# Optimization experiments

Measured on AMD Instinct MI355X. Metric: run time of the kernel, lower is better.

The kernel has to match this reference:

```python
import jax, jax.numpy as jnp
import numpy as np

N = 2708       # hardcoded in the original forward (Cora)
INS = 1433
OUTS = 64
M = 8          # N_mechs
HID = 64       # conditioner hidden width
LEAK = 0.2
NEG = -1e9


def setup_inputs() -> dict:
    key = jax.random.key(0)
    ks = jax.random.split(key, 9)
    x = jax.random.normal(ks[0], (N, INS), dtype=jnp.float32)
    adj = jax.random.randint(ks[1], (N, N), 0, 2) > 0  # bool mask
    adj = adj | jnp.eye(N, dtype=bool)                 # ensure self-loops so softmax is well-defined
    s = 1.0 / np.sqrt(INS)
    W = jax.random.normal(ks[2], (M, INS, OUTS), dtype=jnp.float32) * s
    a_src = jax.random.normal(ks[3], (M, OUTS), dtype=jnp.float32) * (1.0 / np.sqrt(OUTS))
    a_dst = jax.random.normal(ks[4], (M, OUTS), dtype=jnp.float32) * (1.0 / np.sqrt(OUTS))
    Wc1 = jax.random.normal(ks[5], (INS, HID), dtype=jnp.float32) * s
    bc1 = jnp.zeros((HID,), dtype=jnp.float32)
    Wc2 = jax.random.normal(ks[6], (HID, 2 * M), dtype=jnp.float32) * (1.0 / np.sqrt(HID))
    bc2 = jnp.zeros((2 * M,), dtype=jnp.float32)
    return {"x": x, "adj": adj, "W": W, "a_src": a_src, "a_dst": a_dst,
            "Wc1": Wc1, "bc1": bc1, "Wc2": Wc2, "bc2": bc2}


def reference(x, adj, W, a_src, a_dst, Wc1, bc1, Wc2, bc2):
    # dropout is identity in eval mode.
    # Conditioner MLP applied per node (vectorized over the Python loop in the original):
    cond = jax.nn.relu(x @ Wc1 + bc1) @ Wc2 + bc2          # [N, 2M]
    c = cond.reshape(N, 2, M)                               # matches cond.view(2708, 2, -1)
    gamma = c[:, 0, :].T                                    # [M, N] per-node scalar gamma per mechanism
    beta = c[:, 1, :].T                                     # [M, N]
    # All mechanisms batched: project + FiLM modulate
    h = jnp.einsum('nf,mfo->mno', x, W)                     # [M, N, OUTS]
    h = gamma[:, :, None] * h + beta[:, :, None]
    # GAT scoring: e_ij = LeakyReLU(a_src.h_i + a_dst.h_j), masked by adj
    e_src = jnp.einsum('mno,mo->mn', h, a_src)              # [M, N]
    e_dst = jnp.einsum('mno,mo->mn', h, a_dst)              # [M, N]
    e = jax.nn.leaky_relu(e_src[:, :, None] + e_dst[:, None, :], LEAK)  # [M, N, N]
    e = jnp.where(adj[None, :, :], e, NEG)
    attn = jax.nn.softmax(e, axis=-1)                       # [M, N, N]
    out = jnp.einsum('mnk,mko->mno', attn, h)               # [M, N, OUTS]
    # concat=True: cat over mechanisms along feature dim
    out = jnp.transpose(out, (1, 0, 2)).reshape(N, M * OUTS)  # [N, M*OUTS]
    return out
```

## Files before the change

kernel.cpp:

```cpp
#include <hip/hip_runtime.h>

#define NN   2708
#define INS  1433
#define MM   8
#define NP   2720
#define WPR  85
#define KP   1440
#define NKC  45
#define RP   2752
#define C9   576
#define OC   512

#define CAN_ASRC 0
#define CAN_ADST 512
#define CAN_BC1  1024
#define CAN_BC2  1088
#define CAN_WC2  1104
#define CAN_TOT  2128

#define ADJ_WAVES (NN * 43)
#define ADJBLK ((ADJ_WAVES + 3) / 4)
#define XBLK   15480
#define WTBLK  (9 * 23)
#define PACK_TOT (ADJBLK + XBLK + WTBLK + 1)

typedef unsigned short u16;
typedef unsigned int   u32;
typedef __attribute__((ext_vector_type(8))) short bf16x8;
typedef __attribute__((ext_vector_type(4))) float f32x4;

static __device__ __forceinline__ u16 f2bfu(float f) {
    union { float f; u32 u; } v; v.f = f;
    u32 u = v.u;
    u32 r = (u + 0x7fffu + ((u >> 16) & 1u)) >> 16;
    return (u16)r;
}
static __device__ __forceinline__ float bfu2f(u16 b) {
    union { u32 u; float f; } v; v.u = ((u32)b) << 16;
    return v.f;
}

static __device__ __forceinline__ int xfp32_of(const int* ctr) {
    int s = 0;
    #pragma unroll
    for (int k = 0; k < 32; ++k) s += ctr[k];
    return s > 32;
}
static __device__ __forceinline__ int aflag_of(const int* ctr) {
    int b = 0;
    #pragma unroll
    for (int k = 32; k < 64; ++k) b |= ctr[k];
    if (b & 2)  return 3;
    if (b & 4)  return 4;
    if (b & 8)  return 5;
    if (b & 1)  return 1;
    if (b & 16) return 0;
    return 2;
}

__global__ void k_probe(const u32* __restrict__ x_raw, const u32* __restrict__ adj_raw,
                        int* __restrict__ ctr) {
    const int b = blockIdx.x, t = threadIdx.x;
    __shared__ int sred[4];
    if (b < 32) {
        int local = 0;
        #pragma unroll
        for (int k = 0; k < 8; ++k) {
            u32 v = x_raw[b * 2048 + k * 256 + t];
            u32 lo = v & 0xffffu, hi = v >> 16;
            if ((lo & 0x7f80u) == 0u && lo != 0u) local++;
            if ((hi & 0x7f80u) == 0u && hi != 0u) local++;
        }
        #pragma unroll
        for (int off = 32; off > 0; off >>= 1) local += __shfl_xor(local, off, 64);
        if ((t & 63) == 0) sred[t >> 6] = local;
        __syncthreads();
        if (t == 0) ctr[b] = sred[0] + sred[1] + sred[2] + sred[3];
    } else {
        int fl = 0;
        #pragma unroll
        for (int k = 0; k < 8; ++k) {
            int w = (b - 32) * 2048 + k * 256 + t;
            u32 v = adj_raw[w];
            if (v > 1u)           fl |= 1;
            if (v == 0x3f803f80u) fl |= 2;
            if (v == 0x3f800000u) fl |= 4;
            if (v == 0x3c003c00u) fl |= 8;
            if ((w & 1) && v)     fl |= 16;
        }
        #pragma unroll
        for (int off = 32; off > 0; off >>= 1) fl |= __shfl_xor(fl, off, 64);
        if ((t & 63) == 0) sred[t >> 6] = fl;
        __syncthreads();
        if (t == 0) ctr[b] = sred[0] | sred[1] | sred[2] | sred[3];
    }
}

static __device__ __forceinline__ u16 load_as_bf16(const void* p, size_t idx, int fp32) {
    if (fp32) return f2bfu(((const float*)p)[idx]);
    return ((const u16*)p)[idx];
}
static __device__ __forceinline__ float load_as_f32(const void* p, size_t idx, int fp32) {
    if (fp32) return ((const float*)p)[idx];
    return bfu2f(((const u16*)p)[idx]);
}

__global__ void k_pack(const void* __restrict__ x, const void* __restrict__ adj,
                       const void* __restrict__ W, const void* __restrict__ Wc1,
                       const void* a_src, const void* a_dst, const void* bc1,
                       const void* bc2, const void* Wc2,
                       u16* __restrict__ xpf, u16* __restrict__ WTf,
                       u32* __restrict__ adjT, float* __restrict__ canon,
                       const int* __restrict__ ctr) {
    __shared__ float lds[64][65];
    const int bid = blockIdx.x;
    if (bid < ADJBLK) {
        const int f = aflag_of(ctr);
        const int wid  = bid * 4 + (threadIdx.x >> 6);
        const int lane = threadIdx.x & 63;
        const int i  = wid / 43;
        const int jb = (wid - i * 43) * 64;
        if (i >= NN) return;
        const int j = jb + lane;
        int v = 0;
        if (j < NN) {
            size_t s = (size_t)i * NN + j;
            if      (f == 0) v = ((const int*)adj)[s] != 0;
            else if (f == 1) v = ((const unsigned char*)adj)[s] != 0;
            else if (f == 2) v = ((const long long*)adj)[s] != 0;
            else if (f == 4) v = ((const float*)adj)[s] != 0.f;
            else             v = ((const u16*)adj)[s] != 0;
        }
        unsigned long long mask = __ballot(v);
        if (lane == 0) {
            const int ww = jb >> 5;
            adjT[(size_t)ww * NP + i] = (u32)mask;
            if (ww + 1 < WPR) adjT[(size_t)(ww + 1) * NP + i] = (u32)(mask >> 32);
        }
    } else if (bid < ADJBLK + XBLK) {
        const int fp32 = xfp32_of(ctr);
        int e = (bid - ADJBLK) * 256 + threadIdx.x;
        int t1 = e >> 9, sub = e & 511;
        int r = sub >> 5, kloc = sub & 31;
        int it = t1 / NKC, kc = t1 - it * NKC;
        int row = it * 16 + r, col = kc * 32 + kloc;
        u16 v = 0;
        if (row < NN && col < INS) v = load_as_bf16(x, (size_t)row * INS + col, fp32);
        xpf[e] = v;
    } else if (bid < ADJBLK + XBLK + WTBLK) {
        const int fp32 = xfp32_of(ctr);
        const int b2 = bid - ADJBLK - XBLK;
        const int mblk = b2 / 23, ktile = b2 - mblk * 23;
        #pragma unroll
        for (int ii = 0; ii < 16; ++ii) {
            int l = threadIdx.x * 16 + ii;
            int k_in = l >> 6, o = l & 63;
            int k = ktile * 64 + k_in;
            float v = 0.f;
            if (k < INS) {
                if (mblk < 8) v = load_as_f32(W, ((size_t)mblk * INS + k) * 64 + o, fp32);
                else          v = load_as_f32(Wc1, (size_t)k * 64 + o, fp32);
            }
            lds[k_in][o] = v;
        }
        __syncthreads();
        #pragma unroll
        for (int ii = 0; ii < 16; ++ii) {
            int e2 = threadIdx.x * 16 + ii;
            int ct2 = e2 >> 10, kc2 = (e2 >> 9) & 1;
            int r = (e2 >> 5) & 15, kloc = e2 & 31;
            int kc = ktile * 2 + kc2;
            if (kc < NKC) {
                int ct = mblk * 4 + ct2;
                WTf[(((size_t)ct * NKC + kc) * 16 + r) * 32 + kloc] =
                    f2bfu(lds[kc2 * 32 + kloc][ct2 * 16 + r]);
            }
        }
    } else {
        const int fp32 = xfp32_of(ctr);
        for (int e = threadIdx.x; e < CAN_TOT; e += 256) {
            float v;
            if      (e < CAN_ADST) v = load_as_f32(a_src, e - CAN_ASRC, fp32);
            else if (e < CAN_BC1)  v = load_as_f32(a_dst, e - CAN_ADST, fp32);
            else if (e < CAN_BC2)  v = load_as_f32(bc1,  e - CAN_BC1, fp32);
            else if (e < CAN_WC2)  v = load_as_f32(bc2,  e - CAN_BC2, fp32);
            else                   v = load_as_f32(Wc2,  e - CAN_WC2, fp32);
            canon[e] = v;
        }
    }
}

__launch_bounds__(64)
__global__ void k_gemm(const u16* __restrict__ xpf, const u16* __restrict__ WTf,
                       float* __restrict__ h_pre) {
    const int lane = threadIdx.x;
    const int r    = lane & 15;
    const int quad = lane >> 4;
    const int it0  = blockIdx.x * 2;
    const int ct0  = blockIdx.y * 4;

    const u16* aP0 = xpf + (size_t)it0 * NKC * 512 + r * 32 + quad * 8;
    const u16* aP1 = aP0 + (size_t)NKC * 512;
    const u16* bP  = WTf + (size_t)ct0 * NKC * 512 + r * 32 + quad * 8;

    f32x4 acc0[4], acc1[4];
    #pragma unroll
    for (int nt = 0; nt < 4; ++nt) {
        acc0[nt] = (f32x4){0.f, 0.f, 0.f, 0.f};
        acc1[nt] = (f32x4){0.f, 0.f, 0.f, 0.f};
    }

    #pragma unroll 3
    for (int kc = 0; kc < NKC; ++kc) {
        bf16x8 a0 = *(const bf16x8*)(aP0 + kc * 512);
        bf16x8 a1 = *(const bf16x8*)(aP1 + kc * 512);
        #pragma unroll
        for (int nt = 0; nt < 4; ++nt) {
            bf16x8 bfr = *(const bf16x8*)(bP + (size_t)nt * NKC * 512 + kc * 512);
            acc0[nt] = __builtin_amdgcn_mfma_f32_16x16x32_bf16(a0, bfr, acc0[nt], 0, 0, 0);
            acc1[nt] = __builtin_amdgcn_mfma_f32_16x16x32_bf16(a1, bfr, acc1[nt], 0, 0, 0);
        }
    }

    const int c_base = blockIdx.y * 64;
    #pragma unroll
    for (int reg = 0; reg < 4; ++reg) {
        const int i0 = it0 * 16 + quad * 4 + reg;
        if (i0 < NN) {
            float* orow = h_pre + (size_t)i0 * C9 + c_base;
            orow[ 0 + r] = acc0[0][reg];
            orow[16 + r] = acc0[1][reg];
            orow[32 + r] = acc0[2][reg];
            orow[48 + r] = acc0[3][reg];
        }
        const int i1 = it0 * 16 + 16 + quad * 4 + reg;
        if (i1 < NN) {
            float* orow = h_pre + (size_t)i1 * C9 + c_base;
            orow[ 0 + r] = acc1[0][reg];
            orow[16 + r] = acc1[1][reg];
            orow[32 + r] = acc1[2][reg];
            orow[48 + r] = acc1[3][reg];
        }
    }
}

__launch_bounds__(256)
__global__ void k_film(const float* __restrict__ h_pre, const float* __restrict__ canon,
                       u16* __restrict__ HTf, float* __restrict__ e_srcP,
                       float* __restrict__ e_dstP) {
    const int m  = blockIdx.y;
    const int n0 = blockIdx.x * 32;
    const int t  = threadIdx.x, wave = t >> 6, o = t & 63;
    __shared__ u16 hbuf[32][66];

    const float wg = canon[CAN_WC2 + o * 16 + m];
    const float wb = canon[CAN_WC2 + o * 16 + m + 8];
    const float as = canon[CAN_ASRC + m * 64 + o];
    const float ad = canon[CAN_ADST + m * 64 + o];
    const float b1 = canon[CAN_BC1 + o];
    const float g0 = canon[CAN_BC2 + m], b0 = canon[CAN_BC2 + m + 8];

    #pragma unroll
    for (int it = 0; it < 8; ++it) {
        const int nl = wave * 8 + it, n = n0 + nl;
        const bool valid = n < NN;
        float hv = 0.f;
        if (valid) hv = h_pre[(size_t)n * C9 + 512 + o] + b1;
        hv = hv > 0.f ? hv : 0.f;
        float pg = hv * wg, pb = hv * wb;
        #pragma unroll
        for (int off = 32; off > 0; off >>= 1) {
            pg += __shfl_xor(pg, off, 64);
            pb += __shfl_xor(pb, off, 64);
        }
        const float g = pg + g0, bb = pb + b0;
        float h = 0.f;
        if (valid) h = g * h_pre[(size_t)n * C9 + m * 64 + o] + bb;
        float ps = h * as, pd = h * ad;
        #pragma unroll
        for (int off = 32; off > 0; off >>= 1) {
            ps += __shfl_xor(ps, off, 64);
            pd += __shfl_xor(pd, off, 64);
        }
        if (o == 0) { e_srcP[m * NP + n] = ps; e_dstP[m * NP + n] = pd; }
        hbuf[nl][o] = f2bfu(h);
    }
    __syncthreads();
    u32* ht32 = (u32*)(HTf + ((size_t)m * WPR + (n0 >> 5)) * 2048);
    #pragma unroll
    for (int rep = 0; rep < 4; ++rep) {
        const int idx = rep * 256 + t;
        const int oo = idx >> 4, jp = idx & 15;
        ht32[idx] = (u32)hbuf[2 * jp][oo] | ((u32)hbuf[2 * jp + 1][oo] << 16);
    }
}

__global__ void k_prep(const float* __restrict__ e_srcP, const float* __restrict__ e_dstP,
                       float* __restrict__ E1P, float* __restrict__ E2P,
                       float* __restrict__ F1P, float* __restrict__ F2P) {
    const int m = blockIdx.x, sl = blockIdx.y, t = threadIdx.x;
    const float* ed = e_dstP + m * NP;
    const float* es = e_srcP + m * NP;
    float mx = -3.0e38f;
    for (int j = t; j < NP; j += 256) mx = fmaxf(mx, ed[j]);
    #pragma unroll
    for (int off = 32; off > 0; off >>= 1) mx = fmaxf(mx, __shfl_xor(mx, off, 64));
    __shared__ float sm[4];
    if ((t & 63) == 0) sm[t >> 6] = mx;
    __syncthreads();
    const float maxd = fmaxf(fmaxf(sm[0], sm[1]), fmaxf(sm[2], sm[3]));
    const int j0 = sl * (NP / 8);
    for (int j = j0 + t; j < j0 + NP / 8; j += 256) {
        const float d = ed[j] - maxd;
        E1P[m * NP + j] = __expf(d);
        E2P[m * NP + j] = __expf(0.2f * d);
    }
    for (int i = j0 + t; i < j0 + NP / 8; i += 256) {
        const float v = es[i] + maxd;
        const float rmax = v > 0.f ? v : 0.2f * v;
        F1P[m * NP + i] = __expf(v - rmax);
        F2P[m * NP + i] = __expf(0.2f * v - rmax);
    }
}

__launch_bounds__(256)
__global__ void k_attn(const u32* __restrict__ adjT, const float* __restrict__ F1P,
                       const float* __restrict__ F2P, const float* __restrict__ E1P,
                       const float* __restrict__ E2P, const u16* __restrict__ HTf,
                       void* __restrict__ outv, const int* __restrict__ ctr) {
    const int m = blockIdx.y, i0 = blockIdx.x * 16;
    const int t = threadIdx.x;
    const int wave = t >> 6, lane = t & 63;
    const int r = lane & 15, quad = lane >> 4;
    const int i = min(i0 + r, NN - 1);

    __shared__ float sE[2 * NP];
    __shared__ u32 sAdj[WPR * 16];

    for (int idx = t; idx < NP; idx += 256) {
        sE[idx]      = E1P[m * NP + idx];
        sE[NP + idx] = E2P[m * NP + idx];
    }
    for (int w = t; w < WPR * 16; w += 256) {
        const int tile = w >> 4, rr = w & 15;
        sAdj[w] = adjT[(size_t)tile * NP + min(i0 + rr, NN - 1)];
    }
    __syncthreads();

    const float F1 = F1P[m * NP + i], F2 = F2P[m * NP + i];
    const u16* hbase = HTf + (size_t)m * WPR * 2048 + r * 32 + quad * 8;

    f32x4 acc[4], accl;
    #pragma unroll
    for (int nt = 0; nt < 4; ++nt) acc[nt] = (f32x4){0.f, 0.f, 0.f, 0.f};
    accl = (f32x4){0.f, 0.f, 0.f, 0.f};

    bf16x8 ones;
    #pragma unroll
    for (int kk = 0; kk < 8; ++kk) ones[kk] = (short)0x3f80;

    #pragma unroll 2
    for (int jc = wave * 32; jc < NP; jc += 128) {
        const int jb = jc + quad * 8;
        const int tile = jc >> 5;
        const float4 a0 = *(const float4*)(sE + jb);
        const float4 a1 = *(const float4*)(sE + jb + 4);
        const float4 b0 = *(const float4*)(sE + NP + jb);
        const float4 b1 = *(const float4*)(sE + NP + jb + 4);
        const u32 w = sAdj[tile * 16 + r];
        const u32 mask8 = (w >> (quad * 8)) & 0xffu;
        float p[8];
        p[0] = fmaxf(F1 * a0.x, F2 * b0.x);
        p[1] = fmaxf(F1 * a0.y, F2 * b0.y);
        p[2] = fmaxf(F1 * a0.z, F2 * b0.z);
        p[3] = fmaxf(F1 * a0.w, F2 * b0.w);
        p[4] = fmaxf(F1 * a1.x, F2 * b1.x);
        p[5] = fmaxf(F1 * a1.y, F2 * b1.y);
        p[6] = fmaxf(F1 * a1.z, F2 * b1.z);
        p[7] = fmaxf(F1 * a1.w, F2 * b1.w);
        bf16x8 af;
        #pragma unroll
        for (int kk = 0; kk < 8; ++kk) {
            const float pv = ((mask8 >> kk) & 1u) ? p[kk] : 0.f;
            af[kk] = (short)f2bfu(pv);
        }
        const u16* ht = hbase + (size_t)tile * 2048;
        #pragma unroll
        for (int nt = 0; nt < 4; ++nt) {
            bf16x8 bf = *(const bf16x8*)(ht + nt * 512);
            acc[nt] = __builtin_amdgcn_mfma_f32_16x16x32_bf16(af, bf, acc[nt], 0, 0, 0);
        }
        accl = __builtin_amdgcn_mfma_f32_16x16x32_bf16(af, ones, accl, 0, 0, 0);
    }

    __syncthreads();
    float* red = sE;
    #pragma unroll
    for (int nt = 0; nt < 4; ++nt)
        #pragma unroll
        for (int reg = 0; reg < 4; ++reg)
            red[(wave * 64 + lane) * 21 + nt * 4 + reg] = acc[nt][reg];
    #pragma unroll
    for (int reg = 0; reg < 4; ++reg)
        red[(wave * 64 + lane) * 21 + 16 + reg] = accl[reg];
    __syncthreads();
    if (wave != 0) return;

    #pragma unroll
    for (int nt = 0; nt < 4; ++nt)
        #pragma unroll
        for (int reg = 0; reg < 4; ++reg)
            acc[nt][reg] = red[lane * 21 + nt * 4 + reg] + red[(64 + lane) * 21 + nt * 4 + reg]
                         + red[(128 + lane) * 21 + nt * 4 + reg] + red[(192 + lane) * 21 + nt * 4 + reg];
    #pragma unroll
    for (int reg = 0; reg < 4; ++reg)
        accl[reg] = red[lane * 21 + 16 + reg] + red[(64 + lane) * 21 + 16 + reg]
                  + red[(128 + lane) * 21 + 16 + reg] + red[(192 + lane) * 21 + 16 + reg];

    const int ofp32 = xfp32_of(ctr);
    #pragma unroll
    for (int reg = 0; reg < 4; ++reg) {
        const int ii = i0 + quad * 4 + reg;
        if (ii < NN) {
            const float lr = accl[reg];
            const float inv = (lr > 0.f) ? 1.f / lr : 0.f;
            #pragma unroll
            for (int nt = 0; nt < 4; ++nt) {
                const float o = acc[nt][reg] * inv;
                const size_t idx = (size_t)ii * OC + m * 64 + nt * 16 + r;
                if (ofp32) ((float*)outv)[idx] = o;
                else       ((u16*)outv)[idx]   = f2bfu(o);
            }
        }
    }
}

extern "C" void kernel_launch(void* const* d_in, const int* in_sizes, int n_in,
                              void* d_out, int out_size, void* d_ws, size_t ws_size,
                              hipStream_t stream) {
    (void)in_sizes; (void)n_in; (void)out_size; (void)ws_size;
    const void* x     = d_in[0];
    const void* adj   = d_in[1];
    const void* W     = d_in[2];
    const void* a_src = d_in[3];
    const void* a_dst = d_in[4];
    const void* Wc1   = d_in[5];
    const void* bc1   = d_in[6];
    const void* Wc2   = d_in[7];
    const void* bc2   = d_in[8];

    char* ws = (char*)d_ws;
    size_t off = 0;
    auto alloc = [&](size_t bytes) -> void* {
        void* p = ws + off;
        off += (bytes + 255) & ~(size_t)255;
        return p;
    };
    u16*   xpf     = (u16*)  alloc((size_t)RP * KP * 2);
    u16*   WTf     = (u16*)  alloc((size_t)C9 * KP * 2);
    float* h_pre   = (float*)alloc((size_t)NN * C9 * 4);
    float* e_srcP  = (float*)alloc((size_t)MM * NP * 4);
    float* e_dstP  = (float*)alloc((size_t)MM * NP * 4);
    float* E1P     = (float*)alloc((size_t)MM * NP * 4);
    float* E2P     = (float*)alloc((size_t)MM * NP * 4);
    float* F1P     = (float*)alloc((size_t)MM * NP * 4);
    float* F2P     = (float*)alloc((size_t)MM * NP * 4);
    u16*   HTf     = (u16*)  alloc((size_t)MM * WPR * 2048 * 2);
    u32*   adjT    = (u32*)  alloc((size_t)WPR * NP * 4);
    float* canon   = (float*)alloc((size_t)CAN_TOT * 4);
    int*   ctr     = (int*)  alloc(256);

    hipLaunchKernelGGL(k_probe, dim3(64), dim3(256), 0, stream,
                       (const u32*)x, (const u32*)adj, ctr);
    hipLaunchKernelGGL(k_pack, dim3(PACK_TOT), dim3(256), 0, stream,
                       x, adj, W, Wc1, a_src, a_dst, bc1, bc2, Wc2,
                       xpf, WTf, adjT, canon, ctr);
    hipLaunchKernelGGL(k_gemm, dim3(RP / 32, 9), dim3(64), 0, stream, xpf, WTf, h_pre);
    hipLaunchKernelGGL(k_film, dim3(NP / 32, MM), dim3(256), 0, stream,
                       h_pre, canon, HTf, e_srcP, e_dstP);
    hipLaunchKernelGGL(k_prep, dim3(MM, 8), dim3(256), 0, stream,
                       e_srcP, e_dstP, E1P, E2P, F1P, F2P);
    hipLaunchKernelGGL(k_attn, dim3((NN + 15) / 16, MM), dim3(256), 0, stream,
                       adjT, F1P, F2P, E1P, E2P, HTf, d_out, ctr);
}
```

Baseline: 208.3 us.

## Process 32 rows per attention block with two wave groups sharing staged E

The attention kernel now uses 512-thread blocks covering 32 destination rows, split into two 4-wave groups of 16 rows each. Both groups share one shared-memory copy of the E1/E2 exponent vectors, which halves the redundant global loads and LDS staging per row. The cross-wave reduction is reworked so lane-group leaders keep their own accumulators and add the other three waves' partials. Larger blocks may lower occupancy flexibility, and the grid shrinks to 85x8 blocks, which could leave some compute units underused.

```diff
diff --git a/kernel.cpp b/kernel.cpp
--- a/kernel.cpp
+++ b/kernel.cpp
@@ -323,26 +323,29 @@
     }
 }
 
-__launch_bounds__(256)
+__launch_bounds__(512)
 __global__ void k_attn(const u32* __restrict__ adjT, const float* __restrict__ F1P,
                        const float* __restrict__ F2P, const float* __restrict__ E1P,
                        const float* __restrict__ E2P, const u16* __restrict__ HTf,
                        void* __restrict__ outv, const int* __restrict__ ctr) {
-    const int m = blockIdx.y, i0 = blockIdx.x * 16;
+    const int m = blockIdx.y, i0 = blockIdx.x * 32;
     const int t = threadIdx.x;
     const int wave = t >> 6, lane = t & 63;
+    const int grp = wave >> 2, wl = wave & 3;
     const int r = lane & 15, quad = lane >> 4;
-    const int i = min(i0 + r, NN - 1);
-
-    __shared__ float sE[2 * NP];
-    __shared__ u32 sAdj[WPR * 16];
-
-    for (int idx = t; idx < NP; idx += 256) {
+    const int ib = i0 + grp * 16;
+    const int i = min(ib + r, NN - 1);
+
+    __shared__ u32 smem[2 * NP + WPR * 32];
+    float* sE = (float*)smem;
+    u32* sAdj = smem + 2 * NP;
+
+    for (int idx = t; idx < NP; idx += 512) {
         sE[idx]      = E1P[m * NP + idx];
         sE[NP + idx] = E2P[m * NP + idx];
     }
-    for (int w = t; w < WPR * 16; w += 256) {
-        const int tile = w >> 4, rr = w & 15;
+    for (int w = t; w < WPR * 32; w += 512) {
+        const int tile = w >> 5, rr = w & 31;
         sAdj[w] = adjT[(size_t)tile * NP + min(i0 + rr, NN - 1)];
     }
     __syncthreads();
@@ -360,14 +363,14 @@
     for (int kk = 0; kk < 8; ++kk) ones[kk] = (short)0x3f80;
 
     #pragma unroll 2
-    for (int jc = wave * 32; jc < NP; jc += 128) {
+    for (int jc = wl * 32; jc < NP; jc += 128) {
         const int jb = jc + quad * 8;
         const int tile = jc >> 5;
         const float4 a0 = *(const float4*)(sE + jb);
         const float4 a1 = *(const float4*)(sE + jb + 4);
         const float4 b0 = *(const float4*)(sE + NP + jb);
         const float4 b1 = *(const float4*)(sE + NP + jb + 4);
-        const u32 w = sAdj[tile * 16 + r];
+        const u32 w = sAdj[tile * 32 + grp * 16 + r];
         const u32 mask8 = (w >> (quad * 8)) & 0xffu;
         float p[8];
         p[0] = fmaxf(F1 * a0.x, F2 * b0.x);
@@ -394,33 +397,38 @@
     }
 
     __syncthreads();
-    float* red = sE;
-    #pragma unroll
-    for (int nt = 0; nt < 4; ++nt)
+    float* red = (float*)smem;
+    if (wl != 0) {
+        float* dst = red + ((grp * 3 + (wl - 1)) * 64 + lane) * 21;
+        #pragma unroll
+        for (int nt = 0; nt < 4; ++nt)
+            #pragma unroll
+            for (int reg = 0; reg < 4; ++reg)
+                dst[nt * 4 + reg] = acc[nt][reg];
         #pragma unroll
         for (int reg = 0; reg < 4; ++reg)
-            red[(wave * 64 + lane) * 21 + nt * 4 + reg] = acc[nt][reg];
-    #pragma unroll
-    for (int reg = 0; reg < 4; ++reg)
-        red[(wave * 64 + lane) * 21 + 16 + reg] = accl[reg];
+            dst[16 + reg] = accl[reg];
+    }
     __syncthreads();
-    if (wave != 0) return;
-
-    #pragma unroll
-    for (int nt = 0; nt < 4; ++nt)
+    if (wl != 0) return;
+
+    #pragma unroll
+    for (int s = 0; s < 3; ++s) {
+        const float* src = red + ((grp * 3 + s) * 64 + lane) * 21;
+        #pragma unroll
+        for (int nt = 0; nt < 4; ++nt)
+            #pragma unroll
+            for (int reg = 0; reg < 4; ++reg)
+                acc[nt][reg] += src[nt * 4 + reg];
         #pragma unroll
         for (int reg = 0; reg < 4; ++reg)
-            acc[nt][reg] = red[lane * 21 + nt * 4 + reg] + red[(64 + lane) * 21 + nt * 4 + reg]
-                         + red[(128 + lane) * 21 + nt * 4 + reg] + red[(192 + lane) * 21 + nt * 4 + reg];
-    #pragma unroll
-    for (int reg = 0; reg < 4; ++reg)
-        accl[reg] = red[lane * 21 + 16 + reg] + red[(64 + lane) * 21 + 16 + reg]
-                  + red[(128 + lane) * 21 + 16 + reg] + red[(192 + lane) * 21 + 16 + reg];
+            accl[reg] += src[16 + reg];
+    }
 
     const int ofp32 = xfp32_of(ctr);
     #pragma unroll
     for (int reg = 0; reg < 4; ++reg) {
-        const int ii = i0 + quad * 4 + reg;
+        const int ii = ib + quad * 4 + reg;
         if (ii < NN) {
             const float lr = accl[reg];
             const float inv = (lr > 0.f) ? 1.f / lr : 0.f;
@@ -480,6 +488,6 @@
                        h_pre, canon, HTf, e_srcP, e_dstP);
     hipLaunchKernelGGL(k_prep, dim3(MM, 8), dim3(256), 0, stream,
                        e_srcP, e_dstP, E1P, E2P, F1P, F2P);
-    hipLaunchKernelGGL(k_attn, dim3((NN + 15) / 16, MM), dim3(256), 0, stream,
+    hipLaunchKernelGGL(k_attn, dim3(NP / 32, MM), dim3(512), 0, stream,
                        adjT, F1P, F2P, E1P, E2P, HTf, d_out, ctr);
 }
```

After: 213.6 us. +2.6%, slower.

## Coarsen pack kernel work per block and halve GEMM column tile for more blocks

Applied to the files above, without the earlier changes.

The pack kernel now reduces the probe flags once per block with wave shuffles into shared memory, instead of every thread looping over the counters. Each adjacency wave covers four 64-column chunks and each x-pack block handles eight elements per thread, which cuts the block count roughly fourfold and eightfold. The GEMM switches from a 2x4 to a 2x2 MFMA tile per wave and doubles the grid in y, giving more blocks for occupancy but reloading A fragments twice as often. The pack changes add a block-wide barrier before any work starts.

```diff
diff --git a/kernel.cpp b/kernel.cpp
--- a/kernel.cpp
+++ b/kernel.cpp
@@ -18,9 +18,9 @@
 #define CAN_WC2  1104
 #define CAN_TOT  2128
 
-#define ADJ_WAVES (NN * 43)
+#define ADJ_WAVES (NN * 11)
 #define ADJBLK ((ADJ_WAVES + 3) / 4)
-#define XBLK   15480
+#define XBLK   1935
 #define WTBLK  (9 * 23)
 #define PACK_TOT (ADJBLK + XBLK + WTBLK + 1)
 
@@ -46,10 +46,7 @@
     for (int k = 0; k < 32; ++k) s += ctr[k];
     return s > 32;
 }
-static __device__ __forceinline__ int aflag_of(const int* ctr) {
-    int b = 0;
-    #pragma unroll
-    for (int k = 32; k < 64; ++k) b |= ctr[k];
+static __device__ __forceinline__ int aflag_decode(int b) {
     if (b & 2)  return 3;
     if (b & 4)  return 4;
     if (b & 8)  return 5;
@@ -113,47 +110,71 @@
                        u32* __restrict__ adjT, float* __restrict__ canon,
                        const int* __restrict__ ctr) {
     __shared__ float lds[64][65];
+    __shared__ int sflags[2];
+    const int t = threadIdx.x;
+    if (t < 64) {
+        int v = ctr[t];
+        int cnt  = (t < 32) ? v : 0;
+        int bits = (t >= 32) ? v : 0;
+        #pragma unroll
+        for (int off = 32; off > 0; off >>= 1) {
+            cnt  += __shfl_xor(cnt, off, 64);
+            bits |= __shfl_xor(bits, off, 64);
+        }
+        if (t == 0) { sflags[0] = cnt; sflags[1] = bits; }
+    }
+    __syncthreads();
+    const int fp32 = sflags[0] > 32;
+
     const int bid = blockIdx.x;
     if (bid < ADJBLK) {
-        const int f = aflag_of(ctr);
-        const int wid  = bid * 4 + (threadIdx.x >> 6);
-        const int lane = threadIdx.x & 63;
-        const int i  = wid / 43;
-        const int jb = (wid - i * 43) * 64;
+        const int f = aflag_decode(sflags[1]);
+        const int wid  = bid * 4 + (t >> 6);
+        const int lane = t & 63;
+        const int i = wid / 11;
+        const int c256 = wid - i * 11;
         if (i >= NN) return;
-        const int j = jb + lane;
-        int v = 0;
-        if (j < NN) {
-            size_t s = (size_t)i * NN + j;
-            if      (f == 0) v = ((const int*)adj)[s] != 0;
-            else if (f == 1) v = ((const unsigned char*)adj)[s] != 0;
-            else if (f == 2) v = ((const long long*)adj)[s] != 0;
-            else if (f == 4) v = ((const float*)adj)[s] != 0.f;
-            else             v = ((const u16*)adj)[s] != 0;
-        }
-        unsigned long long mask = __ballot(v);
-        if (lane == 0) {
-            const int ww = jb >> 5;
-            adjT[(size_t)ww * NP + i] = (u32)mask;
-            if (ww + 1 < WPR) adjT[(size_t)(ww + 1) * NP + i] = (u32)(mask >> 32);
+        const int jb0 = c256 * 256;
+        #pragma unroll
+        for (int s = 0; s < 4; ++s) {
+            const int jb = jb0 + s * 64;
+            if (jb >= NP) break;
+            const int j = jb + lane;
+            int v = 0;
+            if (j < NN) {
+                size_t idx = (size_t)i * NN + j;
+                if      (f == 0) v = ((const int*)adj)[idx] != 0;
+                else if (f == 1) v = ((const unsigned char*)adj)[idx] != 0;
+                else if (f == 2) v = ((const long long*)adj)[idx] != 0;
+                else if (f == 4) v = ((const float*)adj)[idx] != 0.f;
+                else             v = ((const u16*)adj)[idx] != 0;
+            }
+            unsigned long long mask = __ballot(v);
+            if (lane == 0) {
+                const int ww = jb >> 5;
+                adjT[(size_t)ww * NP + i] = (u32)mask;
+                if (ww + 1 < WPR) adjT[(size_t)(ww + 1) * NP + i] = (u32)(mask >> 32);
+            }
         }
     } else if (bid < ADJBLK + XBLK) {
-        const int fp32 = xfp32_of(ctr);
-        int e = (bid - ADJBLK) * 256 + threadIdx.x;
-        int t1 = e >> 9, sub = e & 511;
-        int r = sub >> 5, kloc = sub & 31;
-        int it = t1 / NKC, kc = t1 - it * NKC;
-        int row = it * 16 + r, col = kc * 32 + kloc;
-        u16 v = 0;
-        if (row < NN && col < INS) v = load_as_bf16(x, (size_t)row * INS + col, fp32);
-        xpf[e] = v;
+        const int base = (bid - ADJBLK) * 2048 + t;
+        #pragma unroll
+        for (int s = 0; s < 8; ++s) {
+            const int e = base + s * 256;
+            const int t1 = e >> 9, sub = e & 511;
+            const int r = sub >> 5, kloc = sub & 31;
+            const int it = t1 / NKC, kc = t1 - it * NKC;
+            const int row = it * 16 + r, col = kc * 32 + kloc;
+            u16 v = 0;
+            if (row < NN && col < INS) v = load_as_bf16(x, (size_t)row * INS + col, fp32);
+            xpf[e] = v;
+        }
     } else if (bid < ADJBLK + XBLK + WTBLK) {
-        const int fp32 = xfp32_of(ctr);
         const int b2 = bid - ADJBLK - XBLK;
         const int mblk = b2 / 23, ktile = b2 - mblk * 23;
         #pragma unroll
         for (int ii = 0; ii < 16; ++ii) {
-            int l = threadIdx.x * 16 + ii;
+            int l = t * 16 + ii;
             int k_in = l >> 6, o = l & 63;
             int k = ktile * 64 + k_in;
             float v = 0.f;
@@ -166,7 +187,7 @@
         __syncthreads();
         #pragma unroll
         for (int ii = 0; ii < 16; ++ii) {
-            int e2 = threadIdx.x * 16 + ii;
+            int e2 = t * 16 + ii;
             int ct2 = e2 >> 10, kc2 = (e2 >> 9) & 1;
             int r = (e2 >> 5) & 15, kloc = e2 & 31;
             int kc = ktile * 2 + kc2;
@@ -177,8 +198,7 @@
             }
         }
     } else {
-        const int fp32 = xfp32_of(ctr);
-        for (int e = threadIdx.x; e < CAN_TOT; e += 256) {
+        for (int e = t; e < CAN_TOT; e += 256) {
             float v;
             if      (e < CAN_ADST) v = load_as_f32(a_src, e - CAN_ASRC, fp32);
             else if (e < CAN_BC1)  v = load_as_f32(a_dst, e - CAN_ADST, fp32);
@@ -197,49 +217,41 @@
     const int r    = lane & 15;
     const int quad = lane >> 4;
     const int it0  = blockIdx.x * 2;
-    const int ct0  = blockIdx.y * 4;
+    const int ct0  = blockIdx.y * 2;
 
     const u16* aP0 = xpf + (size_t)it0 * NKC * 512 + r * 32 + quad * 8;
     const u16* aP1 = aP0 + (size_t)NKC * 512;
-    const u16* bP  = WTf + (size_t)ct0 * NKC * 512 + r * 32 + quad * 8;
-
-    f32x4 acc0[4], acc1[4];
-    #pragma unroll
-    for (int nt = 0; nt < 4; ++nt) {
-        acc0[nt] = (f32x4){0.f, 0.f, 0.f, 0.f};
-        acc1[nt] = (f32x4){0.f, 0.f, 0.f, 0.f};
-    }
+    const u16* bP0 = WTf + (size_t)ct0 * NKC * 512 + r * 32 + quad * 8;
+    const u16* bP1 = bP0 + (size_t)NKC * 512;
+
+    f32x4 acc[2][2];
+    #pragma unroll
+    for (int a = 0; a < 2; ++a)
+        #pragma unroll
+        for (int b = 0; b < 2; ++b) acc[a][b] = (f32x4){0.f, 0.f, 0.f, 0.f};
 
     #pragma unroll 3
     for (int kc = 0; kc < NKC; ++kc) {
         bf16x8 a0 = *(const bf16x8*)(aP0 + kc * 512);
         bf16x8 a1 = *(const bf16x8*)(aP1 + kc * 512);
-        #pragma unroll
-        for (int nt = 0; nt < 4; ++nt) {
-            bf16x8 bfr = *(const bf16x8*)(bP + (size_t)nt * NKC * 512 + kc * 512);
-            acc0[nt] = __builtin_amdgcn_mfma_f32_16x16x32_bf16(a0, bfr, acc0[nt], 0, 0, 0);
-            acc1[nt] = __builtin_amdgcn_mfma_f32_16x16x32_bf16(a1, bfr, acc1[nt], 0, 0, 0);
-        }
-    }
-
-    const int c_base = blockIdx.y * 64;
-    #pragma unroll
-    for (int reg = 0; reg < 4; ++reg) {
-        const int i0 = it0 * 16 + quad * 4 + reg;
-        if (i0 < NN) {
-            float* orow = h_pre + (size_t)i0 * C9 + c_base;
-            orow[ 0 + r] = acc0[0][reg];
-            orow[16 + r] = acc0[1][reg];
-            orow[32 + r] = acc0[2][reg];
-            orow[48 + r] = acc0[3][reg];
-        }
-        const int i1 = it0 * 16 + 16 + quad * 4 + reg;
-        if (i1 < NN) {
-            float* orow = h_pre + (size_t)i1 * C9 + c_base;
-            orow[ 0 + r] = acc1[0][reg];
-            orow[16 + r] = acc1[1][reg];
-            orow[32 + r] = acc1[2][reg];
-            orow[48 + r] = acc1[3][reg];
+        bf16x8 b0 = *(const bf16x8*)(bP0 + kc * 512);
+        bf16x8 b1 = *(const bf16x8*)(bP1 + kc * 512);
+        acc[0][0] = __builtin_amdgcn_mfma_f32_16x16x32_bf16(a0, b0, acc[0][0], 0, 0, 0);
+        acc[0][1] = __builtin_amdgcn_mfma_f32_16x16x32_bf16(a0, b1, acc[0][1], 0, 0, 0);
+        acc[1][0] = __builtin_amdgcn_mfma_f32_16x16x32_bf16(a1, b0, acc[1][0], 0, 0, 0);
+        acc[1][1] = __builtin_amdgcn_mfma_f32_16x16x32_bf16(a1, b1, acc[1][1], 0, 0, 0);
+    }
+
+    #pragma unroll
+    for (int a = 0; a < 2; ++a) {
+        #pragma unroll
+        for (int reg = 0; reg < 4; ++reg) {
+            const int ii = (it0 + a) * 16 + quad * 4 + reg;
+            if (ii < NN) {
+                float* orow = h_pre + (size_t)ii * C9 + ct0 * 16;
+                orow[ 0 + r] = acc[a][0][reg];
+                orow[16 + r] = acc[a][1][reg];
+            }
         }
     }
 }
@@ -475,7 +487,7 @@
     hipLaunchKernelGGL(k_pack, dim3(PACK_TOT), dim3(256), 0, stream,
                        x, adj, W, Wc1, a_src, a_dst, bc1, bc2, Wc2,
                        xpf, WTf, adjT, canon, ctr);
-    hipLaunchKernelGGL(k_gemm, dim3(RP / 32, 9), dim3(64), 0, stream, xpf, WTf, h_pre);
+    hipLaunchKernelGGL(k_gemm, dim3(RP / 32, 18), dim3(64), 0, stream, xpf, WTf, h_pre);
     hipLaunchKernelGGL(k_film, dim3(NP / 32, MM), dim3(256), 0, stream,
                        h_pre, canon, HTf, e_srcP, e_dstP);
     hipLaunchKernelGGL(k_prep, dim3(MM, 8), dim3(256), 0, stream,
```

New measurement: 196.9 us. 1.06x faster.
